# Kernel tuning notes

Hardware: AMD Instinct MI355X
Metric: run time of the kernel (lower is better)

The kernel has to match this reference:

```python
import jax, jax.numpy as jnp
import numpy as np
from jax import lax

B, C_IN, H_IN, W_IN = 128, 256, 8, 32
RH, RW = 16, 64            # rec-head resolution
YOH, XOH = RH // 2, RW // 2  # onehot sizes (8, 32)
HID = 256
NC = 163                   # num classes == embed size
T = 32                     # target length
C_ENC = C_IN + XOH + YOH   # 296 encoder channels
L = (RH // 2) * (RW // 2)  # 256 attention positions


def setup_inputs() -> dict:
    key = jax.random.key(0)
    ks = jax.random.split(key, 18)
    s = 0.05
    return {
        "x": jax.random.normal(ks[0], (B, C_IN, H_IN, W_IN), jnp.float32),
        "decoder_targets": jax.random.randint(ks[1], (B, T), 0, NC),
        "word_targets": jax.random.randint(ks[2], (B, T), 0, NC),
        # seq_encoder conv 3x3
        "conv_w": jax.random.normal(ks[3], (C_IN, C_IN, 3, 3), jnp.float32) * 0.02,
        "conv_b": jnp.zeros((C_IN,), jnp.float32),
        # decoder embedding (post kaiming re-init => random, not identity)
        "emb_dec": jax.random.normal(ks[4], (NC, NC), jnp.float32) * s,
        "word_w": jax.random.normal(ks[5], (HID, NC), jnp.float32) * s,
        "word_b": jnp.zeros((HID,), jnp.float32),
        "attn_w": jax.random.normal(ks[6], (HID, 2 * HID + XOH + YOH), jnp.float32) * s,
        "attn_b": jnp.zeros((HID,), jnp.float32),
        "attn_v": jax.random.normal(ks[7], (HID,), jnp.float32) * (1.0 / np.sqrt(HID)),
        # GRUCell, gate order [r, z, n]
        "gru_wih": jax.random.normal(ks[8], (3 * HID, 2 * HID + XOH + YOH), jnp.float32) * s,
        "gru_bih": jnp.zeros((3 * HID,), jnp.float32),
        "gru_whh": jax.random.normal(ks[9], (3 * HID, HID), jnp.float32) * s,
        "gru_bhh": jnp.zeros((3 * HID,), jnp.float32),
        "out_w": jax.random.normal(ks[10], (NC, HID), jnp.float32) * s,
        "out_b": jnp.zeros((NC,), jnp.float32),
        # positional one-hot embedding tables (also kaiming re-initialized)
        "x_emb": jax.random.normal(ks[11], (XOH, XOH), jnp.float32) * s,
        "y_emb": jax.random.normal(ks[12], (YOH, YOH), jnp.float32) * s,
    }


def _forward(x, conv_w, conv_b, emb_dec, word_w, word_b, attn_w, attn_b, attn_v,
             gru_wih, gru_bih, gru_whh, gru_bhh, out_w, out_b, x_emb, y_emb,
             decoder_targets, word_targets):
    b = x.shape[0]
    # rescale: bilinear upsample (align_corners=False ~ half-pixel)
    xr = jax.image.resize(x, (b, C_IN, RH, RW), method="linear")
    # seq_encoder: conv3x3 + ReLU + maxpool2
    conv = lax.conv_general_dilated(xr, conv_w, (1, 1), "SAME",
                                    dimension_numbers=("NCHW", "OIHW", "NCHW"))
    conv = jax.nn.relu(conv + conv_b[None, :, None, None])
    pooled = lax.reduce_window(conv, -jnp.inf, lax.max,
                               (1, 1, 2, 2), (1, 1, 2, 2), "VALID")  # (B,256,8,32)
    hf, wf = RH // 2, RW // 2
    # positional channels: x_map[c,y,x] = x_emb[x,c]; y_map[c,y,x] = y_emb[y,c]
    x_map = jnp.broadcast_to(x_emb.T[:, None, :], (XOH, hf, wf))
    y_map = jnp.broadcast_to(y_emb.T[:, :, None], (YOH, hf, wf))
    x_map = jnp.broadcast_to(x_map[None], (b, XOH, hf, wf))
    y_map = jnp.broadcast_to(y_map[None], (b, YOH, hf, wf))
    feat = jnp.concatenate([pooled, x_map, y_map], axis=1)      # (B,296,8,32)
    enc = feat.reshape(b, C_ENC, hf * wf).transpose(0, 2, 1)    # (B, L, C)

    t_len = decoder_targets.shape[1]
    # teacher forcing: input at step 0 is BOS (=0), else previous target
    inputs_seq = jnp.concatenate(
        [jnp.zeros((b, 1), decoder_targets.dtype), decoder_targets[:, :-1]], axis=1)

    def step(hidden, xs):
        tok, tgt = xs
        we = emb_dec[tok] @ word_w.T + word_b                   # (B, HID)
        # Bahdanau attention
        hrep = jnp.broadcast_to(hidden[:, None, :], (b, enc.shape[1], HID))
        cat = jnp.concatenate([hrep, enc], axis=-1)             # (B,L,2H+OH)
        energy = jnp.tanh(jnp.einsum("blc,hc->blh", cat, attn_w) + attn_b)
        scores = jnp.einsum("blh,h->bl", energy, attn_v)
        w = jax.nn.softmax(scores, axis=1)                      # (B,L)
        ctx = jnp.einsum("bl,blc->bc", w, enc)                  # (B, C)
        rin = jnp.concatenate([we, ctx], axis=-1)               # (B, 2H+OH)
        # GRUCell
        gi = rin @ gru_wih.T + gru_bih
        gh = hidden @ gru_whh.T + gru_bhh
        i_r, i_z, i_n = jnp.split(gi, 3, axis=-1)
        h_r, h_z, h_n = jnp.split(gh, 3, axis=-1)
        r = jax.nn.sigmoid(i_r + h_r)
        z = jax.nn.sigmoid(i_z + h_z)
        n = jnp.tanh(i_n + r * h_n)
        h_new = (1.0 - z) * n + z * hidden
        logp = jax.nn.log_softmax(h_new @ out_w.T + out_b, axis=1)
        # NLLLoss(ignore_index=-1, reduction='none')
        nll = -jnp.take_along_axis(logp, jnp.clip(tgt, 0)[:, None], axis=1)[:, 0]
        nll = jnp.where(tgt >= 0, nll, 0.0)
        return h_new, nll

    h0 = jnp.zeros((b, HID), jnp.float32)
    _, nlls = lax.scan(step, h0, (inputs_seq.T, word_targets.T))  # (T, B)
    loss_vec = nlls.sum(axis=0)                                   # (B,)
    return 0.2 * (loss_vec.sum() / loss_vec.shape[0])


def reference(x, decoder_targets, word_targets, conv_w, conv_b, emb_dec,
              word_w, word_b, attn_w, attn_b, attn_v, gru_wih, gru_bih,
              gru_whh, gru_bhh, out_w, out_b, x_emb, y_emb):
    return _forward(x, conv_w, conv_b, emb_dec, word_w, word_b, attn_w, attn_b,
                    attn_v, gru_wih, gru_bih, gru_whh, gru_bhh, out_w, out_b,
                    x_emb, y_emb, decoder_targets, word_targets)
```

## Files before the change

kernel.cpp:

```cpp
#include <hip/hip_runtime.h>
#include <hip/hip_bf16.h>
#include <math.h>

#define B    128
#define CIN  256
#define HIN  8
#define WIN_ 32
#define RH   16
#define RW   64
#define HID  256
#define NC   163
#define T    32
#define L    256
#define CENC 296

typedef __attribute__((ext_vector_type(8))) short short8;
typedef __attribute__((ext_vector_type(8))) unsigned short u16x8;
typedef __attribute__((ext_vector_type(4))) float f32x4;

__device__ __forceinline__ float bf2f(unsigned short u) {
    unsigned int x = ((unsigned int)u) << 16;
    return __uint_as_float(x);
}
__device__ __forceinline__ unsigned short f2bf(float f) {
    unsigned int x = __float_as_uint(f);
    unsigned int r = (x + 0x7FFFu + ((x >> 16) & 1u)) >> 16;
    return (unsigned short)r;
}
__device__ __forceinline__ float fast_tanh(float x) {
    float e = __expf(2.f * x);
    return 1.f - 2.f * __builtin_amdgcn_rcpf(e + 1.f);
}
__device__ __forceinline__ float fast_sigm(float x) {
    return __builtin_amdgcn_rcpf(1.f + __expf(-x));
}
__device__ __forceinline__ float wave_red_max(float v) {
    #pragma unroll
    for (int o = 32; o > 0; o >>= 1) v = fmaxf(v, __shfl_down(v, o, 64));
    return v;
}
__device__ __forceinline__ float wave_red_sum(float v) {
    #pragma unroll
    for (int o = 32; o > 0; o >>= 1) v += __shfl_down(v, o, 64);
    return v;
}
__device__ __forceinline__ float half_red_sum(float v) {
    #pragma unroll
    for (int o = 16; o > 0; o >>= 1) v += __shfl_down(v, o, 64);
    return v;
}

__global__ void __launch_bounds__(256) k_upsxt(const float* __restrict__ x,
                                               unsigned short* __restrict__ Xt) {
    __shared__ __align__(16) float sf[64 * 2 * 32];
    const int y = blockIdx.x;
    const int b = blockIdx.y;
    const int tid = threadIdx.x;
    float sy = 0.5f * y - 0.25f;
    int yq0 = (y - 1) >> 1;
    float wy = sy - (float)yq0;
    int y0c = min(max(yq0, 0), HIN - 1);
    int y1c = min(max(yq0 + 1, 0), HIN - 1);
    const int xo = tid & 63;
    const int cj = tid >> 6;
    float sx = 0.5f * xo - 0.25f;
    int xq0 = (xo - 1) >> 1;
    float wx = sx - (float)xq0;
    int x0c = min(max(xq0, 0), WIN_ - 1);
    int x1c = min(max(xq0 + 1, 0), WIN_ - 1);
    for (int cc = 0; cc < 4; cc++) {
        __syncthreads();
        #pragma unroll
        for (int i = 0; i < 4; i++) {
            int idx = tid * 4 + i;
            int c = idx >> 4;
            int rowh = (idx >> 3) & 1;
            int part = idx & 7;
            int ysrc = rowh ? y1c : y0c;
            float4 v = *reinterpret_cast<const float4*>(
                x + ((size_t)(b * CIN + cc * 64 + c) * HIN + ysrc) * WIN_ + part * 4);
            *reinterpret_cast<float4*>(sf + ((c * 2 + rowh) * 32 + part * 4)) = v;
        }
        __syncthreads();
        unsigned short ov[16];
        #pragma unroll
        for (int j = 0; j < 16; j++) {
            int c = cj * 16 + j;
            const float* r0 = sf + (c * 2 + 0) * 32;
            const float* r1 = sf + (c * 2 + 1) * 32;
            float v = (1.f - wy) * ((1.f - wx) * r0[x0c] + wx * r0[x1c])
                    +        wy  * ((1.f - wx) * r1[x0c] + wx * r1[x1c]);
            ov[j] = f2bf(v);
        }
        unsigned short* dst = Xt + ((size_t)((b * 16 + y) * 64 + xo)) * 256 + cc * 64 + cj * 16;
        *reinterpret_cast<u16x8*>(dst)     = *reinterpret_cast<u16x8*>(ov);
        *reinterpret_cast<u16x8*>(dst + 8) = *reinterpret_cast<u16x8*>(ov + 8);
    }
}

__global__ void k_wt(const float* __restrict__ conv_w, unsigned short* __restrict__ Wt) {
    int e = blockIdx.x * 256 + threadIdx.x;
    int ci = e & 255;
    int co = (e >> 8) & 255;
    int s  = e >> 16;
    Wt[(size_t)(s * 256 + co) * 256 + ci] = f2bf(conv_w[(size_t)(co * 256 + ci) * 9 + s]);
}

__global__ void __launch_bounds__(256) k_convmm(const unsigned short* __restrict__ Xt,
        const unsigned short* __restrict__ Wt, const float* __restrict__ conv_b,
        unsigned short* __restrict__ enc_bf) {
    __shared__ __align__(16) char smem[34048];
    unsigned short* A_s = (unsigned short*)smem;
    unsigned short* B_s = A_s + 128 * 40;
    float* pool = (float*)smem;
    const int mt = blockIdx.x;
    const int n0 = blockIdx.y * 128;
    const int b = mt >> 3;
    const int y0 = (mt & 7) * 2;
    const int tid = threadIdx.x;
    const int wave = tid >> 6, lane = tid & 63;
    const int mq = (wave & 1) * 64, nq = (wave >> 1) * 64;
    const int lm = lane & 15, lq = lane >> 4;
    f32x4 acc[4][4];
    #pragma unroll
    for (int mi = 0; mi < 4; mi++)
        #pragma unroll
        for (int ni = 0; ni < 4; ni++)
            #pragma unroll
            for (int r = 0; r < 4; r++) acc[mi][ni][r] = 0.f;

    for (int s9 = 0; s9 < 9; s9++) {
        const int ky = s9 / 3, kx = s9 % 3;
        const unsigned short* Wb = Wt + (size_t)s9 * 256 * 256;
        for (int kc = 0; kc < 256; kc += 32) {
            __syncthreads();
            #pragma unroll
            for (int it = 0; it < 2; it++) {
                int s2 = tid + it * 256;
                int pix = s2 >> 2, q4 = s2 & 3;
                int yy = y0 + (pix >> 6) + ky - 1;
                int xx = (pix & 63) + kx - 1;
                u16x8 va = {0, 0, 0, 0, 0, 0, 0, 0};
                if ((unsigned)yy < 16u && (unsigned)xx < 64u)
                    va = *reinterpret_cast<const u16x8*>(
                        Xt + ((size_t)((b * 16 + yy) * 64 + xx)) * 256 + kc + q4 * 8);
                *reinterpret_cast<u16x8*>(A_s + pix * 40 + q4 * 8) = va;
                u16x8 vb = *reinterpret_cast<const u16x8*>(
                    Wb + (size_t)(n0 + pix) * 256 + kc + q4 * 8);
                *reinterpret_cast<u16x8*>(B_s + pix * 40 + q4 * 8) = vb;
            }
            __syncthreads();
            short8 af[4], bfr[4];
            #pragma unroll
            for (int mi = 0; mi < 4; mi++)
                af[mi] = *reinterpret_cast<const short8*>(A_s + (mq + mi * 16 + lm) * 40 + lq * 8);
            #pragma unroll
            for (int ni = 0; ni < 4; ni++)
                bfr[ni] = *reinterpret_cast<const short8*>(B_s + (nq + ni * 16 + lm) * 40 + lq * 8);
            #pragma unroll
            for (int mi = 0; mi < 4; mi++)
                #pragma unroll
                for (int ni = 0; ni < 4; ni++)
                    acc[mi][ni] = __builtin_amdgcn_mfma_f32_16x16x32_bf16(
                        af[mi], bfr[ni], acc[mi][ni], 0, 0, 0);
        }
    }
    __syncthreads();
    #pragma unroll
    for (int mi = 0; mi < 4; mi++) {
        int px0 = mi * 8 + lq * 2;
        #pragma unroll
        for (int ni = 0; ni < 4; ni++) {
            int nl = nq + ni * 16 + lm;
            float pa = fmaxf(acc[mi][ni][0], acc[mi][ni][1]);
            float pb = fmaxf(acc[mi][ni][2], acc[mi][ni][3]);
            pool[((wave & 1) * 32 + px0) * 132 + nl] = pa;
            pool[((wave & 1) * 32 + px0 + 1) * 132 + nl] = pb;
        }
    }
    __syncthreads();
    {
        int base = tid * 16;
        int px = base >> 7;
        int nb = base & 127;
        unsigned short ov[16];
        #pragma unroll
        for (int i = 0; i < 16; i++) {
            int n = nb + i;
            float v = fmaxf(pool[px * 132 + n], pool[(32 + px) * 132 + n]) + conv_b[n0 + n];
            ov[i] = f2bf(fmaxf(v, 0.f));
        }
        unsigned short* dst = enc_bf + ((size_t)b * L + (mt & 7) * 32 + px) * CENC + n0 + nb;
        *reinterpret_cast<u16x8*>(dst)     = *reinterpret_cast<u16x8*>(ov);
        *reinterpret_cast<u16x8*>(dst + 8) = *reinterpret_cast<u16x8*>(ov + 8);
    }
}

__global__ void k_encpos(const float* __restrict__ x_emb, const float* __restrict__ y_emb,
                         unsigned short* __restrict__ enc_bf, unsigned short* __restrict__ pos2t) {
    int b = blockIdx.x, l = threadIdx.x;
    int yl = l >> 5, xl = l & 31;
    unsigned short* e = enc_bf + (size_t)(b * L + l) * CENC + 256;
    #pragma unroll
    for (int c = 0; c < 32; c++) e[c] = f2bf(x_emb[xl * 32 + c]);
    #pragma unroll
    for (int c = 0; c < 8; c++) e[32 + c] = f2bf(y_emb[yl * 8 + c]);
    if (b == 0) {
        #pragma unroll
        for (int c = 0; c < 32; c++) pos2t[c * 256 + l] = f2bf(x_emb[xl * 32 + c]);
        #pragma unroll
        for (int c = 0; c < 8; c++) pos2t[(32 + c) * 256 + l] = f2bf(y_emb[yl * 8 + c]);
    }
}

__global__ void __launch_bounds__(256) k_enct(const unsigned short* __restrict__ enc_bf,
                                              unsigned short* __restrict__ enc_t) {
    __shared__ unsigned short s[64 * 264];
    const int c0 = blockIdx.x * 64;
    const int b = blockIdx.y;
    const int tid = threadIdx.x;
    #pragma unroll
    for (int j = 0; j < 8; j++) {
        u16x8 u = *reinterpret_cast<const u16x8*>(
            enc_bf + ((size_t)b * L + tid) * CENC + c0 + j * 8);
        #pragma unroll
        for (int k = 0; k < 8; k++) s[(j * 8 + k) * 264 + tid] = u[k];
    }
    __syncthreads();
    {
        int c = tid >> 2, lp = tid & 3;
        const unsigned short* row = s + c * 264 + lp * 64;
        unsigned short* dst = enc_t + ((size_t)b * 256 + c0 + c) * L + lp * 64;
        #pragma unroll
        for (int i = 0; i < 8; i++)
            *reinterpret_cast<u16x8*>(dst + i * 8) =
                *reinterpret_cast<const u16x8*>(row + i * 8);
    }
}

__global__ void __launch_bounds__(256) k_etab(const float* __restrict__ emb_dec,
                                              const float* __restrict__ word_w,
                                              const float* __restrict__ word_b,
                                              float* __restrict__ E) {
    __shared__ float er[NC];
    int row = blockIdx.x, tid = threadIdx.x;
    for (int k = tid; k < NC; k += 256) er[k] = emb_dec[(size_t)row * NC + k];
    __syncthreads();
    float a = word_b[tid];
    for (int k = 0; k < NC; k++) a += er[k] * word_w[(size_t)tid * NC + k];
    E[(size_t)row * HID + tid] = a;
}

__global__ void k_prep(const float* __restrict__ attn_w, const float* __restrict__ out_w,
                       unsigned short* __restrict__ wA_bf, unsigned short* __restrict__ ow_bf) {
    int o = blockIdx.x, k = threadIdx.x;
    wA_bf[(size_t)o * 256 + k] = f2bf(attn_w[(size_t)o * 552 + k]);
    if (o < NC) ow_bf[(size_t)o * 256 + k] = f2bf(out_w[(size_t)o * 256 + k]);
}

__global__ void __launch_bounds__(1024) k_wpack(const float* __restrict__ wih,
        const float* __restrict__ whh, unsigned short* __restrict__ WpackC,
        unsigned short* __restrict__ WpackH) {
    const int blk = blockIdx.x;
    const int tid = threadIdx.x;
    unsigned short o[8];
    if (blk < 37) {
        #pragma unroll
        for (int j = 0; j < 8; j++) {
            int k = blk * 8 + j;
            float v = (tid < 768) ? wih[(size_t)tid * 552 + 256 + k] : 0.f;
            o[j] = f2bf(v);
        }
        *reinterpret_cast<u16x8*>(WpackC + ((size_t)blk * 1024 + tid) * 8) =
            *reinterpret_cast<u16x8*>(o);
    } else {
        int it = blk - 37;
        #pragma unroll
        for (int j = 0; j < 8; j++) {
            int k = it * 8 + j;
            float v = (tid < 768) ? whh[(size_t)tid * 256 + k] : 0.f;
            o[j] = f2bf(v);
        }
        *reinterpret_cast<u16x8*>(WpackH + ((size_t)it * 1024 + tid) * 8) =
            *reinterpret_cast<u16x8*>(o);
    }
}

__global__ void __launch_bounds__(768) k_wge(const float* __restrict__ wih,
                                             unsigned short* __restrict__ WgE) {
    int k = blockIdx.x, g = threadIdx.x;
    WgE[(size_t)k * 768 + g] = f2bf(wih[(size_t)g * 552 + k]);
}
__global__ void __launch_bounds__(768) k_gie(const float* __restrict__ E,
                                             const unsigned short* __restrict__ WgE,
                                             const float* __restrict__ bih,
                                             float* __restrict__ giE) {
    __shared__ float er[256];
    int v = blockIdx.x, g = threadIdx.x;
    if (g < 256) er[g] = E[(size_t)v * 256 + g];
    __syncthreads();
    float a = bih[g];
    #pragma unroll 4
    for (int k = 0; k < 256; k++) a += er[k] * bf2f(WgE[(size_t)k * 768 + g]);
    giE[(size_t)v * 768 + g] = a;
}

__global__ void __launch_bounds__(256) k_ep(const unsigned short* __restrict__ enc_bf,
                                            const float* __restrict__ attn_w,
                                            unsigned short* __restrict__ ep_t) {
    __shared__ __align__(16) float eS[16][132];
    __shared__ __align__(16) float wS[16][36];
    const int l0 = blockIdx.x * 128;
    const int h0 = blockIdx.y * 32;
    const int b = blockIdx.z;
    const int tid = threadIdx.x;
    const int hh = tid >> 5, ll = tid & 31;
    float acc[4][4];
    #pragma unroll
    for (int s2 = 0; s2 < 4; s2++)
        #pragma unroll
        for (int r = 0; r < 4; r++) acc[s2][r] = 0.f;
    for (int kc = 0; kc < CENC; kc += 16) {
        const int kn = min(16, CENC - kc);
        __syncthreads();
        #pragma unroll
        for (int it = 0; it < 2; it++) {
            int idx = it * 256 + tid;
            int lq = idx >> 2, kq = idx & 3;
            float v0 = 0.f, v1 = 0.f, v2 = 0.f, v3 = 0.f;
            if (kq * 4 < kn) {
                ushort4 u = *reinterpret_cast<const ushort4*>(
                    enc_bf + (size_t)(b * L + l0 + lq) * CENC + kc + kq * 4);
                v0 = bf2f(u.x); v1 = bf2f(u.y); v2 = bf2f(u.z); v3 = bf2f(u.w);
            }
            eS[kq * 4 + 0][lq] = v0; eS[kq * 4 + 1][lq] = v1;
            eS[kq * 4 + 2][lq] = v2; eS[kq * 4 + 3][lq] = v3;
        }
        if (tid < 128) {
            int hq = tid >> 2, kq = tid & 3;
            float4 v = make_float4(0.f, 0.f, 0.f, 0.f);
            if (kq * 4 < kn)
                v = *reinterpret_cast<const float4*>(attn_w + (size_t)(h0 + hq) * 552 + 256 + kc + kq * 4);
            wS[kq * 4 + 0][hq] = v.x; wS[kq * 4 + 1][hq] = v.y;
            wS[kq * 4 + 2][hq] = v.z; wS[kq * 4 + 3][hq] = v.w;
        }
        __syncthreads();
        #pragma unroll
        for (int k = 0; k < 16; k++) {
            float4 e = *reinterpret_cast<const float4*>(&eS[k][ll * 4]);
            float4 w = *reinterpret_cast<const float4*>(&wS[k][hh * 4]);
            float ev[4] = {e.x, e.y, e.z, e.w};
            float wv[4] = {w.x, w.y, w.z, w.w};
            #pragma unroll
            for (int s2 = 0; s2 < 4; s2++)
                #pragma unroll
                for (int r = 0; r < 4; r++) acc[s2][r] += wv[s2] * ev[r];
        }
    }
    #pragma unroll
    for (int r = 0; r < 4; r++) {
        ushort4 o;
        o.x = f2bf(acc[0][r]); o.y = f2bf(acc[1][r]);
        o.z = f2bf(acc[2][r]); o.w = f2bf(acc[3][r]);
        *reinterpret_cast<ushort4*>(
            ep_t + ((size_t)(b * L) + l0 + ll * 4 + r) * HID + h0 + hh * 4) = o;
    }
}

__global__ void k_init(int* __restrict__ flagH, int* __restrict__ flagS) {
    if (threadIdx.x < B) { flagH[threadIdx.x] = 0; flagS[threadIdx.x] = 0; }
}

__global__ void __launch_bounds__(1024) k_steps(
        const float* __restrict__ giE, const float* __restrict__ bhh,
        const unsigned short* __restrict__ ep_t, const unsigned short* __restrict__ enc_t,
        const unsigned short* __restrict__ wA_bf, const unsigned short* __restrict__ ow_bf,
        const unsigned short* __restrict__ pos2t,
        const unsigned short* __restrict__ WpackC, const unsigned short* __restrict__ WpackH,
        const float* __restrict__ attn_b, const float* __restrict__ attn_v,
        const float* __restrict__ out_b,
        const int* __restrict__ dec_tgt, const int* __restrict__ word_tgt,
        float* __restrict__ nllG,
        unsigned int* __restrict__ hX32, unsigned int* __restrict__ sX32,
        int* __restrict__ flagH, int* __restrict__ flagS) {
    const int bid = blockIdx.x;
    const bool roleA = bid < B;
    const int b = bid & (B - 1);
    const int tid = threadIdx.x;
    const int hwid = tid >> 5, l32 = tid & 31;

    __shared__ __align__(16) unsigned short big[L * 256];
    __shared__ __align__(16) unsigned short rin[552];
    __shared__ __align__(16) unsigned short swl[256];
    __shared__ __align__(16) unsigned short hp[256], vb[256];
    __shared__ float hfS[256];
    __shared__ float scr[256];
    __shared__ float red[16];
    __shared__ float rzS[512], inS[256], hnS[256];
    unsigned int* rin32 = reinterpret_cast<unsigned int*>(rin);
    unsigned int* swl32 = reinterpret_cast<unsigned int*>(swl);

    if (roleA) {
        if (tid < 256) vb[tid] = f2bf(attn_v[tid]);
        {
            const u16x8* src = reinterpret_cast<const u16x8*>(ep_t + (size_t)b * L * 256);
            u16x8* dst = reinterpret_cast<u16x8*>(big);
            #pragma unroll
            for (int i = 0; i < 8; i++) dst[tid + i * 1024] = src[tid + i * 1024];
        }
        float nllacc = 0.f;
        __syncthreads();
        for (int t = 0; t <= T; t++) {
            if (tid == 0) {
                while (__hip_atomic_load(&flagH[b], __ATOMIC_RELAXED,
                                         __HIP_MEMORY_SCOPE_AGENT) < t + 1)
                    __builtin_amdgcn_s_sleep(1);
            }
            __syncthreads();
            if (tid < 128)
                rin32[148 + tid] = __hip_atomic_load(&hX32[b * 128 + tid], __ATOMIC_RELAXED,
                                                     __HIP_MEMORY_SCOPE_AGENT);
            __syncthreads();
            if (t < T) {
                #pragma unroll
                for (int it = 0; it < 8; it++) {
                    int row = it * 32 + hwid;
                    u16x8 w = *reinterpret_cast<const u16x8*>(wA_bf + (size_t)row * 256 + l32 * 8);
                    u16x8 hh = *reinterpret_cast<const u16x8*>(rin + 296 + l32 * 8);
                    float d = 0.f;
                    #pragma unroll
                    for (int j = 0; j < 8; j++) d += bf2f(w[j]) * bf2f(hh[j]);
                    d = half_red_sum(d);
                    if (l32 == 0) hp[row] = f2bf(d + attn_b[row]);
                }
                __syncthreads();
                #pragma unroll
                for (int it = 0; it < 8; it++) {
                    int row = it * 32 + hwid;
                    u16x8 e = *reinterpret_cast<const u16x8*>(big + (size_t)row * 256 + l32 * 8);
                    u16x8 hp8 = *reinterpret_cast<const u16x8*>(hp + l32 * 8);
                    u16x8 vv = *reinterpret_cast<const u16x8*>(vb + l32 * 8);
                    float d = 0.f;
                    #pragma unroll
                    for (int j = 0; j < 8; j++)
                        d += bf2f(vv[j]) * fast_tanh(bf2f(e[j]) + bf2f(hp8[j]));
                    d = half_red_sum(d);
                    if (l32 == 0) scr[row] = d;
                }
                __syncthreads();
                float sc = -1e30f;
                if (tid < 256) {
                    sc = scr[tid];
                    float m = wave_red_max(sc);
                    if ((tid & 63) == 0) red[tid >> 6] = m;
                }
                __syncthreads();
                float M2 = fmaxf(fmaxf(red[0], red[1]), fmaxf(red[2], red[3]));
                float e2 = 0.f;
                if (tid < 256) {
                    e2 = __expf(sc - M2);
                    float sm = wave_red_sum(e2);
                    if ((tid & 63) == 0) red[8 + (tid >> 6)] = sm;
                }
                __syncthreads();
                if (tid < 256) {
                    float invS = __builtin_amdgcn_rcpf(red[8] + red[9] + red[10] + red[11]);
                    swl[tid] = f2bf(e2 * invS);
                }
                __syncthreads();
                if (tid < 128)
                    __hip_atomic_store(&sX32[b * 128 + tid], swl32[tid], __ATOMIC_RELAXED,
                                       __HIP_MEMORY_SCOPE_AGENT);
                __syncthreads();
                if (tid == 0)
                    __hip_atomic_store(&flagS[b], t + 1, __ATOMIC_RELAXED,
                                       __HIP_MEMORY_SCOPE_AGENT);
            }
            if (t > 0) {
                #pragma unroll
                for (int it = 0; it < 6; it++) {
                    int row = it * 32 + hwid;
                    float d = 0.f;
                    if (row < NC) {
                        u16x8 w = *reinterpret_cast<const u16x8*>(ow_bf + (size_t)row * 256 + l32 * 8);
                        u16x8 hh = *reinterpret_cast<const u16x8*>(rin + 296 + l32 * 8);
                        #pragma unroll
                        for (int j = 0; j < 8; j++) d += bf2f(w[j]) * bf2f(hh[j]);
                    }
                    d = half_red_sum(d);
                    if (l32 == 0 && row < NC) scr[row] = d + out_b[row];
                }
                __syncthreads();
                float lg = -1e30f;
                if (tid < 256) {
                    if (tid < NC) lg = scr[tid];
                    float m = wave_red_max(lg);
                    if ((tid & 63) == 0) red[tid >> 6] = m;
                }
                __syncthreads();
                float M = fmaxf(fmaxf(red[0], red[1]), fmaxf(red[2], red[3]));
                if (tid < 256) {
                    float e = (tid < NC) ? __expf(lg - M) : 0.f;
                    float sm = wave_red_sum(e);
                    if ((tid & 63) == 0) red[8 + (tid >> 6)] = sm;
                }
                __syncthreads();
                if (tid == 0) {
                    float S = red[8] + red[9] + red[10] + red[11];
                    int tgt = word_tgt[b * T + (t - 1)];
                    if (tgt >= 0) nllacc += M + __logf(S) - scr[tgt];
                }
                __syncthreads();
            }
        }
        if (tid == 0) nllG[b] = nllacc;
    } else {
        {
            const u16x8* src = reinterpret_cast<const u16x8*>(enc_t + (size_t)b * 256 * 256);
            u16x8* dst = reinterpret_cast<u16x8*>(big);
            #pragma unroll
            for (int i = 0; i < 8; i++) dst[tid + i * 1024] = src[tid + i * 1024];
        }
        __syncthreads();
        for (int t = 0; t <= T; t++) {
            if (tid < 256) {
                float h;
                if (t == 0) {
                    h = 0.f;
                } else {
                    float hold = hfS[tid];
                    int tokp = (t == 1) ? 0 : dec_tgt[b * T + (t - 2)];
                    const float* gE = giE + (size_t)tokp * 768;
                    float r_ = fast_sigm(rzS[tid] + gE[tid] + bhh[tid]);
                    float z_ = fast_sigm(rzS[256 + tid] + gE[256 + tid] + bhh[256 + tid]);
                    float n_ = fast_tanh(inS[tid] + gE[512 + tid] + r_ * (hnS[tid] + bhh[512 + tid]));
                    h = (1.f - z_) * n_ + z_ * hold;
                }
                hfS[tid] = h;
                rin[296 + tid] = f2bf(h);
            }
            __syncthreads();
            if (tid < 128)
                __hip_atomic_store(&hX32[b * 128 + tid], rin32[148 + tid], __ATOMIC_RELAXED,
                                   __HIP_MEMORY_SCOPE_AGENT);
            __syncthreads();
            if (tid == 0)
                __hip_atomic_store(&flagH[b], t + 1, __ATOMIC_RELAXED,
                                   __HIP_MEMORY_SCOPE_AGENT);
            if (t == T) break;
            float hacc = 0.f;
            if (tid < 768) {
                float a0 = 0.f, a1 = 0.f;
                #pragma unroll 4
                for (int it = 0; it < 32; it++) {
                    u16x8 w = *reinterpret_cast<const u16x8*>(WpackH + ((size_t)it * 1024 + tid) * 8);
                    u16x8 r8 = *reinterpret_cast<const u16x8*>(rin + 296 + it * 8);
                    #pragma unroll
                    for (int j = 0; j < 8; j += 2) {
                        a0 += bf2f(w[j]) * bf2f(r8[j]);
                        a1 += bf2f(w[j + 1]) * bf2f(r8[j + 1]);
                    }
                }
                hacc = a0 + a1;
            }
            if (tid == 0) {
                while (__hip_atomic_load(&flagS[b], __ATOMIC_RELAXED,
                                         __HIP_MEMORY_SCOPE_AGENT) < t + 1)
                    __builtin_amdgcn_s_sleep(1);
            }
            __syncthreads();
            if (tid < 128)
                swl32[tid] = __hip_atomic_load(&sX32[b * 128 + tid], __ATOMIC_RELAXED,
                                               __HIP_MEMORY_SCOPE_AGENT);
            __syncthreads();
            #pragma unroll
            for (int it = 0; it < 8; it++) {
                int row = it * 32 + hwid;
                u16x8 e = *reinterpret_cast<const u16x8*>(big + (size_t)row * 256 + l32 * 8);
                u16x8 ss = *reinterpret_cast<const u16x8*>(swl + l32 * 8);
                float d = 0.f;
                #pragma unroll
                for (int j = 0; j < 8; j++) d += bf2f(ss[j]) * bf2f(e[j]);
                d = half_red_sum(d);
                if (l32 == 0) rin[row] = f2bf(d);
            }
            #pragma unroll
            for (int it = 0; it < 2; it++) {
                int row = it * 32 + hwid;
                float d = 0.f;
                if (row < 40) {
                    u16x8 p = *reinterpret_cast<const u16x8*>(pos2t + (size_t)row * 256 + l32 * 8);
                    u16x8 ss = *reinterpret_cast<const u16x8*>(swl + l32 * 8);
                    #pragma unroll
                    for (int j = 0; j < 8; j++) d += bf2f(ss[j]) * bf2f(p[j]);
                }
                d = half_red_sum(d);
                if (l32 == 0 && row < 40) rin[256 + row] = f2bf(d);
            }
            __syncthreads();
            if (tid < 768) {
                float c0 = 0.f, c1 = 0.f;
                #pragma unroll 4
                for (int it = 0; it < 37; it++) {
                    u16x8 w = *reinterpret_cast<const u16x8*>(WpackC + ((size_t)it * 1024 + tid) * 8);
                    u16x8 r8 = *reinterpret_cast<const u16x8*>(rin + it * 8);
                    #pragma unroll
                    for (int j = 0; j < 8; j += 2) {
                        c0 += bf2f(w[j]) * bf2f(r8[j]);
                        c1 += bf2f(w[j + 1]) * bf2f(r8[j + 1]);
                    }
                }
                float cacc = c0 + c1;
                if (tid < 512) rzS[tid] = cacc + hacc;
                else { inS[tid - 512] = cacc; hnS[tid - 512] = hacc; }
            }
            __syncthreads();
        }
    }
}

__global__ void k_reduce(const float* __restrict__ nll, float* __restrict__ out) {
    __shared__ float red[2];
    float v = nll[threadIdx.x];
    v = wave_red_sum(v);
    if ((threadIdx.x & 63) == 0) red[threadIdx.x >> 6] = v;
    __syncthreads();
    if (threadIdx.x == 0) out[0] = 0.2f * (red[0] + red[1]) * (1.f / 128.f);
}

extern "C" void kernel_launch(void* const* d_in, const int* in_sizes, int n_in,
                              void* d_out, int out_size, void* d_ws, size_t ws_size,
                              hipStream_t stream) {
    const float* x        = (const float*)d_in[0];
    const int*   dec_tgt  = (const int*)d_in[1];
    const int*   word_tgt = (const int*)d_in[2];
    const float* conv_w   = (const float*)d_in[3];
    const float* conv_b   = (const float*)d_in[4];
    const float* emb_dec  = (const float*)d_in[5];
    const float* word_w   = (const float*)d_in[6];
    const float* word_b   = (const float*)d_in[7];
    const float* attn_w   = (const float*)d_in[8];
    const float* attn_b   = (const float*)d_in[9];
    const float* attn_v   = (const float*)d_in[10];
    const float* gru_wih  = (const float*)d_in[11];
    const float* gru_bih  = (const float*)d_in[12];
    const float* gru_whh  = (const float*)d_in[13];
    const float* gru_bhh  = (const float*)d_in[14];
    const float* out_w    = (const float*)d_in[15];
    const float* out_b    = (const float*)d_in[16];
    const float* x_emb    = (const float*)d_in[17];
    const float* y_emb    = (const float*)d_in[18];

    char* ws = (char*)d_ws;
    size_t off = 0;
    auto alloc = [&](size_t bytes) -> void* {
        void* p = ws + off;
        off = (off + bytes + 255) & ~(size_t)255;
        return p;
    };
    unsigned short* Xt     = (unsigned short*)alloc((size_t)B * 16 * 64 * 256 * 2);
    unsigned short* enc_bf = (unsigned short*)alloc((size_t)B * L * CENC * 2);
    unsigned short* Wt     = (unsigned short*)alloc((size_t)9 * 256 * 256 * 2);
    float* E      = (float*)alloc((size_t)NC * HID * 4);
    unsigned short* wA_bf  = (unsigned short*)alloc((size_t)HID * HID * 2);
    unsigned short* ow_bf  = (unsigned short*)alloc((size_t)NC * HID * 2);
    unsigned short* WpackC = (unsigned short*)alloc((size_t)37 * 1024 * 8 * 2);
    unsigned short* WpackH = (unsigned short*)alloc((size_t)32 * 1024 * 8 * 2);
    unsigned short* WgE    = (unsigned short*)alloc((size_t)256 * 768 * 2);
    float* giE    = (float*)alloc((size_t)NC * 768 * 4);
    unsigned short* pos2t  = (unsigned short*)alloc((size_t)40 * 256 * 2);
    float* nllG   = (float*)alloc((size_t)B * 4);
    unsigned int* hX32     = (unsigned int*)alloc((size_t)B * 128 * 4);
    unsigned int* sX32     = (unsigned int*)alloc((size_t)B * 128 * 4);
    int* flagH    = (int*)alloc((size_t)B * 4);
    int* flagS    = (int*)alloc((size_t)B * 4);
    unsigned short* ep_t  = Xt;
    unsigned short* enc_t = Xt + (size_t)B * L * HID;
    float* out    = (float*)d_out;

    hipLaunchKernelGGL(k_init, dim3(1), dim3(256), 0, stream, flagH, flagS);
    hipLaunchKernelGGL(k_upsxt, dim3(16, 128), dim3(256), 0, stream, x, Xt);
    hipLaunchKernelGGL(k_wt, dim3(2304), dim3(256), 0, stream, conv_w, Wt);
    hipLaunchKernelGGL(k_encpos, dim3(128), dim3(256), 0, stream, x_emb, y_emb, enc_bf, pos2t);
    hipLaunchKernelGGL(k_convmm, dim3(1024, 2), dim3(256), 0, stream, Xt, Wt, conv_b, enc_bf);
    hipLaunchKernelGGL(k_etab, dim3(163), dim3(256), 0, stream, emb_dec, word_w, word_b, E);
    hipLaunchKernelGGL(k_prep, dim3(256), dim3(256), 0, stream, attn_w, out_w, wA_bf, ow_bf);
    hipLaunchKernelGGL(k_wpack, dim3(69), dim3(1024), 0, stream, gru_wih, gru_whh, WpackC, WpackH);
    hipLaunchKernelGGL(k_wge, dim3(256), dim3(768), 0, stream, gru_wih, WgE);
    hipLaunchKernelGGL(k_gie, dim3(163), dim3(768), 0, stream, E, WgE, gru_bih, giE);
    hipLaunchKernelGGL(k_ep, dim3(2, 8, 128), dim3(256), 0, stream, enc_bf, attn_w, ep_t);
    hipLaunchKernelGGL(k_enct, dim3(4, 128), dim3(256), 0, stream, enc_bf, enc_t);
    hipLaunchKernelGGL(k_steps, dim3(256), dim3(1024), 0, stream,
                       giE, gru_bhh, ep_t, enc_t, wA_bf, ow_bf, pos2t, WpackC, WpackH,
                       attn_b, attn_v, out_b, dec_tgt, word_tgt, nllG,
                       hX32, sX32, flagH, flagS);
    hipLaunchKernelGGL(k_reduce, dim3(1), dim3(128), 0, stream, nllG, out);
}
```

Measured before the change: 1.214 ms.

## Deepen conv GEMM K-tile to 64 and keep GRU recurrent vectors in fp32 LDS

The conv implicit GEMM now stages 64-wide K chunks, with padded rows of 72, and runs two MFMA sub-steps per barrier pair. This halves the number of sync/load rounds. Separately, the persistent recurrent kernel now keeps the hidden state, attention projections and context vector in fp32 shared memory instead of bf16. That removes repeated bf16 unpack and repack in the inner dot products, at the cost of more LDS and wider shared reads. A bf16 mailbox is still used for cross-block exchange.

```diff
diff --git a/kernel.cpp b/kernel.cpp
--- a/kernel.cpp
+++ b/kernel.cpp
@@ -109,9 +109,9 @@
 __global__ void __launch_bounds__(256) k_convmm(const unsigned short* __restrict__ Xt,
         const unsigned short* __restrict__ Wt, const float* __restrict__ conv_b,
         unsigned short* __restrict__ enc_bf) {
-    __shared__ __align__(16) char smem[34048];
+    __shared__ __align__(16) char smem[36864];
     unsigned short* A_s = (unsigned short*)smem;
-    unsigned short* B_s = A_s + 128 * 40;
+    unsigned short* B_s = A_s + 128 * 72;
     float* pool = (float*)smem;
     const int mt = blockIdx.x;
     const int n0 = blockIdx.y * 128;
@@ -132,37 +132,45 @@
     for (int s9 = 0; s9 < 9; s9++) {
         const int ky = s9 / 3, kx = s9 % 3;
         const unsigned short* Wb = Wt + (size_t)s9 * 256 * 256;
-        for (int kc = 0; kc < 256; kc += 32) {
+        for (int kc = 0; kc < 256; kc += 64) {
             __syncthreads();
             #pragma unroll
-            for (int it = 0; it < 2; it++) {
+            for (int it = 0; it < 8; it++) {
                 int s2 = tid + it * 256;
-                int pix = s2 >> 2, q4 = s2 & 3;
-                int yy = y0 + (pix >> 6) + ky - 1;
-                int xx = (pix & 63) + kx - 1;
-                u16x8 va = {0, 0, 0, 0, 0, 0, 0, 0};
-                if ((unsigned)yy < 16u && (unsigned)xx < 64u)
-                    va = *reinterpret_cast<const u16x8*>(
-                        Xt + ((size_t)((b * 16 + yy) * 64 + xx)) * 256 + kc + q4 * 8);
-                *reinterpret_cast<u16x8*>(A_s + pix * 40 + q4 * 8) = va;
-                u16x8 vb = *reinterpret_cast<const u16x8*>(
-                    Wb + (size_t)(n0 + pix) * 256 + kc + q4 * 8);
-                *reinterpret_cast<u16x8*>(B_s + pix * 40 + q4 * 8) = vb;
-            }
-            __syncthreads();
-            short8 af[4], bfr[4];
-            #pragma unroll
-            for (int mi = 0; mi < 4; mi++)
-                af[mi] = *reinterpret_cast<const short8*>(A_s + (mq + mi * 16 + lm) * 40 + lq * 8);
-            #pragma unroll
-            for (int ni = 0; ni < 4; ni++)
-                bfr[ni] = *reinterpret_cast<const short8*>(B_s + (nq + ni * 16 + lm) * 40 + lq * 8);
-            #pragma unroll
-            for (int mi = 0; mi < 4; mi++)
+                int i = s2 & 1023;
+                int row = i >> 3, q8 = i & 7;
+                if (s2 < 1024) {
+                    int yy = y0 + (row >> 6) + ky - 1;
+                    int xx = (row & 63) + kx - 1;
+                    u16x8 va = {0, 0, 0, 0, 0, 0, 0, 0};
+                    if ((unsigned)yy < 16u && (unsigned)xx < 64u)
+                        va = *reinterpret_cast<const u16x8*>(
+                            Xt + ((size_t)((b * 16 + yy) * 64 + xx)) * 256 + kc + q8 * 8);
+                    *reinterpret_cast<u16x8*>(A_s + row * 72 + q8 * 8) = va;
+                } else {
+                    u16x8 vb = *reinterpret_cast<const u16x8*>(
+                        Wb + (size_t)(n0 + row) * 256 + kc + q8 * 8);
+                    *reinterpret_cast<u16x8*>(B_s + row * 72 + q8 * 8) = vb;
+                }
+            }
+            __syncthreads();
+            for (int ks = 0; ks < 2; ks++) {
+                short8 af[4], bfr[4];
+                #pragma unroll
+                for (int mi = 0; mi < 4; mi++)
+                    af[mi] = *reinterpret_cast<const short8*>(
+                        A_s + (mq + mi * 16 + lm) * 72 + ks * 32 + lq * 8);
                 #pragma unroll
                 for (int ni = 0; ni < 4; ni++)
-                    acc[mi][ni] = __builtin_amdgcn_mfma_f32_16x16x32_bf16(
-                        af[mi], bfr[ni], acc[mi][ni], 0, 0, 0);
+                    bfr[ni] = *reinterpret_cast<const short8*>(
+                        B_s + (nq + ni * 16 + lm) * 72 + ks * 32 + lq * 8);
+                #pragma unroll
+                for (int mi = 0; mi < 4; mi++)
+                    #pragma unroll
+                    for (int ni = 0; ni < 4; ni++)
+                        acc[mi][ni] = __builtin_amdgcn_mfma_f32_16x16x32_bf16(
+                            af[mi], bfr[ni], acc[mi][ni], 0, 0, 0);
+            }
         }
     }
     __syncthreads();
@@ -390,18 +398,20 @@
     const int hwid = tid >> 5, l32 = tid & 31;
 
     __shared__ __align__(16) unsigned short big[L * 256];
-    __shared__ __align__(16) unsigned short rin[552];
+    __shared__ __align__(16) unsigned short hmail[256];
     __shared__ __align__(16) unsigned short swl[256];
-    __shared__ __align__(16) unsigned short hp[256], vb[256];
+    __shared__ __align__(16) float rinF[552];
+    __shared__ __align__(16) float hF[256];
+    __shared__ __align__(16) float hpF[256], vbF[256], swlF[256];
     __shared__ float hfS[256];
     __shared__ float scr[256];
     __shared__ float red[16];
     __shared__ float rzS[512], inS[256], hnS[256];
-    unsigned int* rin32 = reinterpret_cast<unsigned int*>(rin);
+    unsigned int* hmail32 = reinterpret_cast<unsigned int*>(hmail);
     unsigned int* swl32 = reinterpret_cast<unsigned int*>(swl);
 
     if (roleA) {
-        if (tid < 256) vb[tid] = f2bf(attn_v[tid]);
+        if (tid < 256) vbF[tid] = attn_v[tid];
         {
             const u16x8* src = reinterpret_cast<const u16x8*>(ep_t + (size_t)b * L * 256);
             u16x8* dst = reinterpret_cast<u16x8*>(big);
@@ -417,33 +427,44 @@
                     __builtin_amdgcn_s_sleep(1);
             }
             __syncthreads();
-            if (tid < 128)
-                rin32[148 + tid] = __hip_atomic_load(&hX32[b * 128 + tid], __ATOMIC_RELAXED,
-                                                     __HIP_MEMORY_SCOPE_AGENT);
+            if (tid < 128) {
+                unsigned int u = __hip_atomic_load(&hX32[b * 128 + tid], __ATOMIC_RELAXED,
+                                                   __HIP_MEMORY_SCOPE_AGENT);
+                hF[2 * tid]     = bf2f((unsigned short)(u & 0xffffu));
+                hF[2 * tid + 1] = bf2f((unsigned short)(u >> 16));
+            }
             __syncthreads();
             if (t < T) {
                 #pragma unroll
                 for (int it = 0; it < 8; it++) {
                     int row = it * 32 + hwid;
                     u16x8 w = *reinterpret_cast<const u16x8*>(wA_bf + (size_t)row * 256 + l32 * 8);
-                    u16x8 hh = *reinterpret_cast<const u16x8*>(rin + 296 + l32 * 8);
-                    float d = 0.f;
-                    #pragma unroll
-                    for (int j = 0; j < 8; j++) d += bf2f(w[j]) * bf2f(hh[j]);
+                    float4 ha = *reinterpret_cast<const float4*>(hF + l32 * 8);
+                    float4 hb = *reinterpret_cast<const float4*>(hF + l32 * 8 + 4);
+                    float d = bf2f(w[0]) * ha.x + bf2f(w[1]) * ha.y
+                            + bf2f(w[2]) * ha.z + bf2f(w[3]) * ha.w
+                            + bf2f(w[4]) * hb.x + bf2f(w[5]) * hb.y
+                            + bf2f(w[6]) * hb.z + bf2f(w[7]) * hb.w;
                     d = half_red_sum(d);
-                    if (l32 == 0) hp[row] = f2bf(d + attn_b[row]);
+                    if (l32 == 0) hpF[row] = d + attn_b[row];
                 }
                 __syncthreads();
                 #pragma unroll
                 for (int it = 0; it < 8; it++) {
                     int row = it * 32 + hwid;
                     u16x8 e = *reinterpret_cast<const u16x8*>(big + (size_t)row * 256 + l32 * 8);
-                    u16x8 hp8 = *reinterpret_cast<const u16x8*>(hp + l32 * 8);
-                    u16x8 vv = *reinterpret_cast<const u16x8*>(vb + l32 * 8);
-                    float d = 0.f;
-                    #pragma unroll
-                    for (int j = 0; j < 8; j++)
-                        d += bf2f(vv[j]) * fast_tanh(bf2f(e[j]) + bf2f(hp8[j]));
+                    float4 ha = *reinterpret_cast<const float4*>(hpF + l32 * 8);
+                    float4 hb = *reinterpret_cast<const float4*>(hpF + l32 * 8 + 4);
+                    float4 va = *reinterpret_cast<const float4*>(vbF + l32 * 8);
+                    float4 vv = *reinterpret_cast<const float4*>(vbF + l32 * 8 + 4);
+                    float d = va.x * fast_tanh(bf2f(e[0]) + ha.x)
+                            + va.y * fast_tanh(bf2f(e[1]) + ha.y)
+                            + va.z * fast_tanh(bf2f(e[2]) + ha.z)
+                            + va.w * fast_tanh(bf2f(e[3]) + ha.w)
+                            + vv.x * fast_tanh(bf2f(e[4]) + hb.x)
+                            + vv.y * fast_tanh(bf2f(e[5]) + hb.y)
+                            + vv.z * fast_tanh(bf2f(e[6]) + hb.z)
+                            + vv.w * fast_tanh(bf2f(e[7]) + hb.w);
                     d = half_red_sum(d);
                     if (l32 == 0) scr[row] = d;
                 }
@@ -483,9 +504,12 @@
                     float d = 0.f;
                     if (row < NC) {
                         u16x8 w = *reinterpret_cast<const u16x8*>(ow_bf + (size_t)row * 256 + l32 * 8);
-                        u16x8 hh = *reinterpret_cast<const u16x8*>(rin + 296 + l32 * 8);
-                        #pragma unroll
-                        for (int j = 0; j < 8; j++) d += bf2f(w[j]) * bf2f(hh[j]);
+                        float4 ha = *reinterpret_cast<const float4*>(hF + l32 * 8);
+                        float4 hb = *reinterpret_cast<const float4*>(hF + l32 * 8 + 4);
+                        d = bf2f(w[0]) * ha.x + bf2f(w[1]) * ha.y
+                          + bf2f(w[2]) * ha.z + bf2f(w[3]) * ha.w
+                          + bf2f(w[4]) * hb.x + bf2f(w[5]) * hb.y
+                          + bf2f(w[6]) * hb.z + bf2f(w[7]) * hb.w;
                     }
                     d = half_red_sum(d);
                     if (l32 == 0 && row < NC) scr[row] = d + out_b[row];
@@ -537,11 +561,12 @@
                     h = (1.f - z_) * n_ + z_ * hold;
                 }
                 hfS[tid] = h;
-                rin[296 + tid] = f2bf(h);
+                hmail[tid] = f2bf(h);
+                rinF[296 + tid] = h;
             }
             __syncthreads();
             if (tid < 128)
-                __hip_atomic_store(&hX32[b * 128 + tid], rin32[148 + tid], __ATOMIC_RELAXED,
+                __hip_atomic_store(&hX32[b * 128 + tid], hmail32[tid], __ATOMIC_RELAXED,
                                    __HIP_MEMORY_SCOPE_AGENT);
             __syncthreads();
             if (tid == 0)
@@ -554,12 +579,12 @@
                 #pragma unroll 4
                 for (int it = 0; it < 32; it++) {
                     u16x8 w = *reinterpret_cast<const u16x8*>(WpackH + ((size_t)it * 1024 + tid) * 8);
-                    u16x8 r8 = *reinterpret_cast<const u16x8*>(rin + 296 + it * 8);
-                    #pragma unroll
-                    for (int j = 0; j < 8; j += 2) {
-                        a0 += bf2f(w[j]) * bf2f(r8[j]);
-                        a1 += bf2f(w[j + 1]) * bf2f(r8[j + 1]);
-                    }
+                    float4 ra = *reinterpret_cast<const float4*>(rinF + 296 + it * 8);
+                    float4 rb = *reinterpret_cast<const float4*>(rinF + 296 + it * 8 + 4);
+                    a0 += bf2f(w[0]) * ra.x + bf2f(w[2]) * ra.z
+                        + bf2f(w[4]) * rb.x + bf2f(w[6]) * rb.z;
+                    a1 += bf2f(w[1]) * ra.y + bf2f(w[3]) * ra.w
+                        + bf2f(w[5]) * rb.y + bf2f(w[7]) * rb.w;
                 }
                 hacc = a0 + a1;
             }
@@ -569,20 +594,25 @@
                     __builtin_amdgcn_s_sleep(1);
             }
             __syncthreads();
-            if (tid < 128)
-                swl32[tid] = __hip_atomic_load(&sX32[b * 128 + tid], __ATOMIC_RELAXED,
-                                               __HIP_MEMORY_SCOPE_AGENT);
+            if (tid < 128) {
+                unsigned int u = __hip_atomic_load(&sX32[b * 128 + tid], __ATOMIC_RELAXED,
+                                                   __HIP_MEMORY_SCOPE_AGENT);
+                swlF[2 * tid]     = bf2f((unsigned short)(u & 0xffffu));
+                swlF[2 * tid + 1] = bf2f((unsigned short)(u >> 16));
+            }
             __syncthreads();
             #pragma unroll
             for (int it = 0; it < 8; it++) {
                 int row = it * 32 + hwid;
                 u16x8 e = *reinterpret_cast<const u16x8*>(big + (size_t)row * 256 + l32 * 8);
-                u16x8 ss = *reinterpret_cast<const u16x8*>(swl + l32 * 8);
-                float d = 0.f;
-                #pragma unroll
-                for (int j = 0; j < 8; j++) d += bf2f(ss[j]) * bf2f(e[j]);
+                float4 sa = *reinterpret_cast<const float4*>(swlF + l32 * 8);
+                float4 sb = *reinterpret_cast<const float4*>(swlF + l32 * 8 + 4);
+                float d = bf2f(e[0]) * sa.x + bf2f(e[1]) * sa.y
+                        + bf2f(e[2]) * sa.z + bf2f(e[3]) * sa.w
+                        + bf2f(e[4]) * sb.x + bf2f(e[5]) * sb.y
+                        + bf2f(e[6]) * sb.z + bf2f(e[7]) * sb.w;
                 d = half_red_sum(d);
-                if (l32 == 0) rin[row] = f2bf(d);
+                if (l32 == 0) rinF[row] = d;
             }
             #pragma unroll
             for (int it = 0; it < 2; it++) {
@@ -590,12 +620,15 @@
                 float d = 0.f;
                 if (row < 40) {
                     u16x8 p = *reinterpret_cast<const u16x8*>(pos2t + (size_t)row * 256 + l32 * 8);
-                    u16x8 ss = *reinterpret_cast<const u16x8*>(swl + l32 * 8);
-                    #pragma unroll
-                    for (int j = 0; j < 8; j++) d += bf2f(ss[j]) * bf2f(p[j]);
+                    float4 sa = *reinterpret_cast<const float4*>(swlF + l32 * 8);
+                    float4 sb = *reinterpret_cast<const float4*>(swlF + l32 * 8 + 4);
+                    d = bf2f(p[0]) * sa.x + bf2f(p[1]) * sa.y
+                      + bf2f(p[2]) * sa.z + bf2f(p[3]) * sa.w
+                      + bf2f(p[4]) * sb.x + bf2f(p[5]) * sb.y
+                      + bf2f(p[6]) * sb.z + bf2f(p[7]) * sb.w;
                 }
                 d = half_red_sum(d);
-                if (l32 == 0 && row < 40) rin[256 + row] = f2bf(d);
+                if (l32 == 0 && row < 40) rinF[256 + row] = d;
             }
             __syncthreads();
             if (tid < 768) {
@@ -603,12 +636,12 @@
                 #pragma unroll 4
                 for (int it = 0; it < 37; it++) {
                     u16x8 w = *reinterpret_cast<const u16x8*>(WpackC + ((size_t)it * 1024 + tid) * 8);
-                    u16x8 r8 = *reinterpret_cast<const u16x8*>(rin + it * 8);
-                    #pragma unroll
-                    for (int j = 0; j < 8; j += 2) {
-                        c0 += bf2f(w[j]) * bf2f(r8[j]);
-                        c1 += bf2f(w[j + 1]) * bf2f(r8[j + 1]);
-                    }
+                    float4 ra = *reinterpret_cast<const float4*>(rinF + it * 8);
+                    float4 rb = *reinterpret_cast<const float4*>(rinF + it * 8 + 4);
+                    c0 += bf2f(w[0]) * ra.x + bf2f(w[2]) * ra.z
+                        + bf2f(w[4]) * rb.x + bf2f(w[6]) * rb.z;
+                    c1 += bf2f(w[1]) * ra.y + bf2f(w[3]) * ra.w
+                        + bf2f(w[5]) * rb.y + bf2f(w[7]) * rb.w;
                 }
                 float cacc = c0 + c1;
                 if (tid < 512) rzS[tid] = cacc + hacc;
```

After: 1.253 ms. 1.03x slower.
